# Optimization experiments

Measured on AMD Instinct MI355X. Metric: run time of the kernel, lower is better.

Reference implementation:

```python
import jax, jax.numpy as jnp
import numpy as np
from jax import lax

B, C, H, W = 8, 128, 64, 64
L = H * W  # 4096, multiple of 64 so BiMamba2's pad-to-chunk is a no-op
DM, DI, DS, DC, NH, HD = 32, 64, 64, 4, 1, 64  # d_model, d_inner, d_state, d_conv, nheads, headdim


def setup_inputs() -> dict:
    key = jax.random.key(0)
    ks = jax.random.split(key, 12)
    def r(i, shape, s):
        return jax.random.normal(ks[i], shape, jnp.float32) * s
    return {
        "x": jax.random.normal(ks[0], (B, C, H, W), jnp.float32),
        "lin1_w": r(1, (C, C), 0.05), "lin1_b": jnp.zeros((C,), jnp.float32),
        "dw_w": r(2, (C, 1, 3, 3), 0.1), "dw_b": jnp.zeros((C,), jnp.float32),
        "fc_in_w": r(3, (C, DM), 0.05),
        "mam_in_w": r(4, (2, DM, 2 * DI + 2 * DS + NH), 0.05),
        "mam_conv_w": r(5, (2, DI + 2 * DS, DC), 0.1),
        "mam_conv_b": jnp.zeros((2, DI + 2 * DS), jnp.float32),
        "mam_dt_bias": r(6, (2, NH), 0.1),
        "mam_A_log": jnp.zeros((2, NH), jnp.float32),
        "mam_D": jnp.ones((2, NH), jnp.float32),
        "mam_norm_w": jnp.ones((2, DI), jnp.float32),
        "mam_out_w": r(7, (2, DI, DM), 0.05),
        "fc_out_w": r(8, (DM, C), 0.05),
        "bn_g": jnp.ones((C,), jnp.float32), "bn_b": jnp.zeros((C,), jnp.float32),
        "conv4_w": r(9, (C, C), 0.05), "conv4_b": jnp.zeros((C,), jnp.float32),
    }


def _causal_dwconv1d(x, w, b):
    # x: (B, L, Ch); w: (Ch, DC) depthwise causal kernel (torch Conv1d groups=Ch, pad=DC-1, trimmed)
    xc = jnp.transpose(x, (0, 2, 1))
    xc = jnp.pad(xc, ((0, 0), (0, 0), (DC - 1, 0)))
    o = lax.conv_general_dilated(xc, w[:, None, :], (1,), "VALID",
                                 feature_group_count=w.shape[0],
                                 dimension_numbers=("NCH", "OIH", "NCH"))
    return jnp.transpose(o + b[None, :, None], (0, 2, 1))


def _mamba2(u, W_in, conv_w, conv_b, dt_bias, A_log, D, norm_w, W_out):
    # u: (B, L, DM). Minimal Mamba2 block: in_proj -> causal dwconv/silu -> selective scan -> gated RMSNorm -> out_proj
    b, l, _ = u.shape
    zxbcdt = u @ W_in                         # (b, l, 2*DI + 2*DS + NH)
    z = zxbcdt[..., :DI]
    xBC = zxbcdt[..., DI:DI + DI + 2 * DS]
    dt = zxbcdt[..., -NH:]
    xBC = jax.nn.silu(_causal_dwconv1d(xBC, conv_w, conv_b))
    xs = xBC[..., :DI]
    Bm = xBC[..., DI:DI + DS]                 # (b, l, DS)
    Cm = xBC[..., DI + DS:]                   # (b, l, DS)
    dt = jax.nn.softplus(dt + dt_bias)        # (b, l, NH)
    dA = jnp.exp(dt * (-jnp.exp(A_log)))      # (b, l, NH)
    xh = xs.reshape(b, l, NH, HD)
    dtx = dt[..., None] * xh                  # (b, l, NH, HD)

    def step(h, inp):
        dA_t, dtx_t, B_t, C_t = inp
        h = dA_t[:, :, None, None] * h + dtx_t[..., None] * B_t[:, None, None, :]
        y = jnp.einsum("bhpn,bn->bhp", h, C_t)
        return h, y

    h0 = jnp.zeros((b, NH, HD, DS), u.dtype)
    _, ys = lax.scan(step, h0, (jnp.moveaxis(dA, 1, 0), jnp.moveaxis(dtx, 1, 0),
                                jnp.moveaxis(Bm, 1, 0), jnp.moveaxis(Cm, 1, 0)))
    y = jnp.moveaxis(ys, 0, 1) + D[None, None, :, None] * xh   # (b, l, NH, HD)
    y = y.reshape(b, l, DI)
    y = y * jax.nn.silu(z)                    # gated RMSNorm
    y = y * lax.rsqrt(jnp.mean(y * y, -1, keepdims=True) + 1e-5) * norm_w
    return y @ W_out                          # (b, l, DM)


def _forward(x, lin1_w, lin1_b, dw_w, dw_b, fc_in_w, mam_in_w, mam_conv_w, mam_conv_b,
             mam_dt_bias, mam_A_log, mam_D, mam_norm_w, mam_out_w, fc_out_w,
             bn_g, bn_b, conv4_w, conv4_b):
    b, c, h, w = x.shape
    o = jnp.einsum("bihw,io->bohw", x, lin1_w) + lin1_b[None, :, None, None]
    o = lax.conv_general_dilated(o, dw_w, (1, 1), "SAME", feature_group_count=c,
                                 dimension_numbers=("NCHW", "OIHW", "NCHW")) + dw_b[None, :, None, None]
    o = jax.nn.silu(o)
    # BiMamba2_2D: flatten HxW -> sequence, fc_in, forward + reversed Mamba2, fc_out
    s = jnp.einsum("bcl,cd->bld", o.reshape(b, c, h * w), fc_in_w)
    y1 = _mamba2(s, mam_in_w[0], mam_conv_w[0], mam_conv_b[0], mam_dt_bias[0],
                 mam_A_log[0], mam_D[0], mam_norm_w[0], mam_out_w[0])
    y2 = jnp.flip(_mamba2(jnp.flip(s, 1), mam_in_w[1], mam_conv_w[1], mam_conv_b[1],
                          mam_dt_bias[1], mam_A_log[1], mam_D[1], mam_norm_w[1], mam_out_w[1]), 1)
    o = jnp.transpose((y1 + y2) @ fc_out_w, (0, 2, 1)).reshape(b, c, h, w)
    # BatchNorm2d (training-mode batch statistics)
    mu = jnp.mean(o, (0, 2, 3), keepdims=True)
    var = jnp.mean((o - mu) ** 2, (0, 2, 3), keepdims=True)
    o = (o - mu) * lax.rsqrt(var + 1e-5) * bn_g[None, :, None, None] + bn_b[None, :, None, None]
    g = jax.nn.sigmoid(jnp.einsum("bihw,io->bohw", o, conv4_w) + conv4_b[None, :, None, None])
    return g * x + x


def reference(x, lin1_w, lin1_b, dw_w, dw_b, fc_in_w, mam_in_w, mam_conv_w, mam_conv_b,
              mam_dt_bias, mam_A_log, mam_D, mam_norm_w, mam_out_w, fc_out_w,
              bn_g, bn_b, conv4_w, conv4_b):
    return _forward(x, lin1_w, lin1_b, dw_w, dw_b, fc_in_w, mam_in_w, mam_conv_w, mam_conv_b,
                    mam_dt_bias, mam_A_log, mam_D, mam_norm_w, mam_out_w, fc_out_w,
                    bn_g, bn_b, conv4_w, conv4_b)
```

## Files before the change

kernel.cpp:

```cpp
#include <hip/hip_runtime.h>
#include <math.h>

constexpr int Bn = 8, Cn = 128, Ln = 4096;

constexpr size_t OFF_O1   = 0;
constexpr size_t OFF_O2   = 4194304;
constexpr size_t OFF_S    = 8388608;
constexpr size_t OFF_Z    = 9437184;
constexpr size_t OFF_WT   = 11534336;
constexpr size_t OFF_XBCA = 13631488;
constexpr size_t OFF_DTS  = 26214400;
constexpr size_t OFF_CUM  = 26279936;
constexpr size_t OFF_T    = 26345472;
constexpr size_t OFF_SPREV= 30539776;
constexpr size_t OFF_S2A  = 34734080;
constexpr size_t OFF_S2B  = 35782656;
constexpr size_t OFF_BN   = 36831232;
constexpr size_t OFF_O3   = 0;

constexpr long XSTRIDE_H = 6291456;
constexpr long TSTRIDE = 2097152;

typedef __attribute__((ext_vector_type(8))) short short8;
typedef __attribute__((ext_vector_type(4))) float f32x4;
typedef __attribute__((ext_vector_type(4))) unsigned short us4;

__device__ __forceinline__ float siluf(float v) { return v / (1.0f + expf(-v)); }

__device__ __forceinline__ unsigned short tobf(float f) {
  unsigned int u = __float_as_uint(f);
  u += 0x7FFFu + ((u >> 16) & 1u);
  return (unsigned short)(u >> 16);
}

__device__ __forceinline__ float frombf(unsigned short u) {
  return __uint_as_float(((unsigned int)u) << 16);
}

__device__ __forceinline__ short8 ldfrag(const unsigned short* p) {
  union { unsigned int u[4]; short8 s; } cv;
  cv.u[0] = *(const unsigned int*)(p);
  cv.u[1] = *(const unsigned int*)(p + 2);
  cv.u[2] = *(const unsigned int*)(p + 4);
  cv.u[3] = *(const unsigned int*)(p + 6);
  return cv.s;
}

__global__ void k_prepW(const float* __restrict__ Win, unsigned short* __restrict__ WT) {
  int dir = blockIdx.x, tid = threadIdx.x;
  for (int idx = tid; idx < 272 * 32; idx += 256) {
    int n = idx >> 5, kk = idx & 31;
    float v = (n < 257) ? Win[dir * 32 * 257 + kk * 257 + n] : 0.f;
    WT[dir * 8704 + idx] = tobf(v);
  }
}

__global__ __launch_bounds__(256) void k_lin1(const float* __restrict__ x,
                                              const float* __restrict__ w,
                                              const float* __restrict__ bias,
                                              float* __restrict__ o1) {
  __shared__ unsigned short wT[64][140];
  __shared__ unsigned short xT[64][140];
  int b = blockIdx.y, l0 = blockIdx.x * 64, cb = blockIdx.z * 64;
  int tid = threadIdx.x, lane = tid & 63, mt = tid >> 6;
  int q = lane >> 4, i = lane & 15;
  int c4 = (tid & 15) * 4, k0 = tid >> 4;
#pragma unroll
  for (int s = 0; s < 8; ++s) {
    int k = k0 + s * 16;
    float4 wv = *(const float4*)&w[k * 128 + cb + c4];
    wT[c4 + 0][k] = tobf(wv.x); wT[c4 + 1][k] = tobf(wv.y);
    wT[c4 + 2][k] = tobf(wv.z); wT[c4 + 3][k] = tobf(wv.w);
    float4 xv = *(const float4*)&x[((long)b * 128 + k) * 4096 + l0 + c4];
    xT[c4 + 0][k] = tobf(xv.x); xT[c4 + 1][k] = tobf(xv.y);
    xT[c4 + 2][k] = tobf(xv.z); xT[c4 + 3][k] = tobf(xv.w);
  }
  __syncthreads();
  short8 af[4];
#pragma unroll
  for (int kk = 0; kk < 4; ++kk)
    af[kk] = ldfrag(&wT[mt * 16 + i][q * 8 + 32 * kk]);
  float bv[4];
#pragma unroll
  for (int r2 = 0; r2 < 4; ++r2) bv[r2] = bias[cb + 16 * mt + q * 4 + r2];
#pragma unroll
  for (int nt = 0; nt < 4; ++nt) {
    f32x4 d = {0.f, 0.f, 0.f, 0.f};
#pragma unroll
    for (int kk = 0; kk < 4; ++kk) {
      short8 bfr = ldfrag(&xT[nt * 16 + i][q * 8 + 32 * kk]);
      d = __builtin_amdgcn_mfma_f32_16x16x32_bf16(af[kk], bfr, d, 0, 0, 0);
    }
#pragma unroll
    for (int r2 = 0; r2 < 4; ++r2) {
      int c = 16 * mt + q * 4 + r2;
      o1[((long)b * 128 + cb + c) * 4096 + l0 + nt * 16 + i] = d[r2] + bv[r2];
    }
  }
}

__global__ void k_dw(const float* __restrict__ o1, const float* __restrict__ wgt,
                     const float* __restrict__ bias, float* __restrict__ o2) {
  __shared__ float p[4096];
  int bc = blockIdx.x, c = bc & 127, tid = threadIdx.x;
  const float* src = o1 + (long)bc * 4096;
#pragma unroll
  for (int s4 = 0; s4 < 4; ++s4) {
    int off = s4 * 1024 + tid * 4;
    *(float4*)&p[off] = *(const float4*)&src[off];
  }
  float wr[9];
#pragma unroll
  for (int j = 0; j < 9; ++j) wr[j] = wgt[c * 9 + j];
  float bv = bias[c];
  __syncthreads();
  int wg = tid & 15, hs = tid >> 4;
  int w0 = wg * 4, h0 = hs * 4;
  float in[6][6];
#pragma unroll
  for (int ri = 0; ri < 6; ++ri) {
    int h = h0 - 1 + ri;
    if (h < 0 || h > 63) {
#pragma unroll
      for (int ci = 0; ci < 6; ++ci) in[ri][ci] = 0.f;
    } else {
      float4 cc = *(float4*)&p[h * 64 + w0];
      in[ri][1] = cc.x; in[ri][2] = cc.y; in[ri][3] = cc.z; in[ri][4] = cc.w;
      in[ri][0] = (w0 > 0) ? p[h * 64 + w0 - 1] : 0.f;
      in[ri][5] = (w0 < 60) ? p[h * 64 + w0 + 4] : 0.f;
    }
  }
#pragma unroll
  for (int r = 0; r < 4; ++r) {
    float oc[4];
#pragma unroll
    for (int q = 0; q < 4; ++q) {
      float acc = bv;
#pragma unroll
      for (int dh = 0; dh < 3; ++dh)
#pragma unroll
        for (int dq = 0; dq < 3; ++dq)
          acc += in[r + dh][q + dq] * wr[dh * 3 + dq];
      oc[q] = siluf(acc);
    }
    *(float4*)&o2[(long)bc * 4096 + (h0 + r) * 64 + w0] =
        make_float4(oc[0], oc[1], oc[2], oc[3]);
  }
}

__global__ void k_fcin(const float* __restrict__ o2, const float* __restrict__ w,
                       unsigned short* __restrict__ sb) {
  __shared__ float xt[128][64];
  __shared__ float wt[128][32];
  int b = blockIdx.y, l0 = blockIdx.x * 64;
  int tid = threadIdx.x;
  int f4 = (tid & 15) * 4, r0 = tid >> 4;
#pragma unroll
  for (int st = 0; st < 8; ++st) {
    int r = r0 + st * 16;
    *(float4*)&xt[r][f4] = *(const float4*)&o2[((long)b * 128 + r) * 4096 + l0 + f4];
  }
  int f4w = (tid & 7) * 4, rw = tid >> 3;
#pragma unroll
  for (int st = 0; st < 4; ++st) {
    int r = rw + st * 32;
    *(float4*)&wt[r][f4w] = *(const float4*)&w[r * 32 + f4w];
  }
  __syncthreads();
  int tx = tid & 15, ty = tid >> 4;
  int c0 = tx * 4, d0 = ty * 2;
  float acc[2][4] = {};
  for (int k = 0; k < 128; ++k) {
    float4 xv = *(float4*)&xt[k][c0];
    float2 wv = *(float2*)&wt[k][d0];
    float xa[4] = {xv.x, xv.y, xv.z, xv.w};
#pragma unroll
    for (int q = 0; q < 4; ++q) {
      acc[0][q] += wv.x * xa[q];
      acc[1][q] += wv.y * xa[q];
    }
  }
#pragma unroll
  for (int q = 0; q < 4; ++q) {
    long ob = ((long)b * 4096 + l0 + c0 + q) * 32 + d0;
    unsigned int pk = (unsigned int)tobf(acc[0][q]) |
                      ((unsigned int)tobf(acc[1][q]) << 16);
    *(unsigned int*)&sb[ob] = pk;
  }
}

__global__ __launch_bounds__(256) void k_inprojconv(
    const unsigned short* __restrict__ sb, const unsigned short* __restrict__ WT,
    const float* __restrict__ conv_w, const float* __restrict__ conv_b,
    const float* __restrict__ dt_bias, const float* __restrict__ A_log,
    unsigned short* __restrict__ zT, unsigned short* __restrict__ xbca,
    float* __restrict__ dts, float* __restrict__ cum) {
  __shared__ unsigned short xbcT[192][82];
  __shared__ float dtL[64];
  int dir = blockIdx.z, b = blockIdx.y, l0 = blockIdx.x * 64;
  int tid = threadIdx.x, lane = tid & 63, mt = tid >> 6;
  int q = lane >> 4, i = lane & 15;
  long rowbase = (long)b * 4096 + l0;
  const unsigned short* W = WT + (long)dir * 8704;
  const short8 zfrag = {0, 0, 0, 0, 0, 0, 0, 0};

  if (mt == 0) {
    short8 afr[4];
#pragma unroll
    for (int rt = 0; rt < 4; ++rt) {
      int l = l0 + 16 * rt + i;
      int lsrc = dir ? (4095 - l) : l;
      afr[rt] = *(const short8*)&sb[((long)b * 4096 + lsrc) * 32 + q * 8];
    }
#pragma unroll
    for (int ct = 0; ct < 4; ++ct) {
      int n = 16 * ct + i;
      short8 bfr = *(const short8*)&W[n * 32 + q * 8];
      unsigned short* zrow = zT + (((long)dir * 64 + n) * 8 + b) * 4096 + l0 + q * 4;
#pragma unroll
      for (int rt = 0; rt < 4; ++rt) {
        f32x4 d = {0.f, 0.f, 0.f, 0.f};
        d = __builtin_amdgcn_mfma_f32_16x16x32_bf16(afr[rt], bfr, d, 0, 0, 0);
        us4 pk;
        pk[0] = tobf(d[0]); pk[1] = tobf(d[1]);
        pk[2] = tobf(d[2]); pk[3] = tobf(d[3]);
        *(us4*)&zrow[16 * rt] = pk;
      }
    }
    {
      short8 bfr = *(const short8*)&W[(256 + i) * 32 + q * 8];
#pragma unroll
      for (int rt = 0; rt < 4; ++rt) {
        f32x4 d = {0.f, 0.f, 0.f, 0.f};
        d = __builtin_amdgcn_mfma_f32_16x16x32_bf16(afr[rt], bfr, d, 0, 0, 0);
        if (i == 0) {
#pragma unroll
          for (int r2 = 0; r2 < 4; ++r2) dtL[16 * rt + q * 4 + r2] = d[r2];
        }
      }
    }
  } else {
    short8 afr[5];
#pragma unroll
    for (int rt = 0; rt < 5; ++rt) {
      int l = l0 - 3 + 16 * rt + i;
      if (l >= 0 && l < 4096) {
        int lsrc = dir ? (4095 - l) : l;
        afr[rt] = *(const short8*)&sb[((long)b * 4096 + lsrc) * 32 + q * 8];
      } else {
        afr[rt] = zfrag;
      }
    }
#pragma unroll
    for (int cti = 0; cti < 4; ++cti) {
      int n = 16 * (mt * 4 + cti) + i;
      short8 bfr = *(const short8*)&W[n * 32 + q * 8];
      int cc = n - 64;
#pragma unroll
      for (int rt = 0; rt < 5; ++rt) {
        f32x4 d = {0.f, 0.f, 0.f, 0.f};
        d = __builtin_amdgcn_mfma_f32_16x16x32_bf16(afr[rt], bfr, d, 0, 0, 0);
        int rr0 = 16 * rt + q * 4;
        unsigned int p0 = (unsigned int)tobf(d[0]) | ((unsigned int)tobf(d[1]) << 16);
        unsigned int p1 = (unsigned int)tobf(d[2]) | ((unsigned int)tobf(d[3]) << 16);
        *(unsigned int*)&xbcT[cc][rr0] = p0;
        *(unsigned int*)&xbcT[cc][rr0 + 2] = p1;
      }
    }
  }
  __syncthreads();

  if (tid < 192) {
    int c = tid;
    float cw0 = conv_w[dir * 768 + c * 4 + 0];
    float cw1 = conv_w[dir * 768 + c * 4 + 1];
    float cw2 = conv_w[dir * 768 + c * 4 + 2];
    float cw3 = conv_w[dir * 768 + c * 4 + 3];
    float cb2 = conv_b[dir * 192 + c];
    unsigned short* xp = xbca + (long)dir * XSTRIDE_H;
    float win0 = 0.f, win1 = 0.f, win2 = 0.f, win3 = 0.f;
    for (int rp = 0; rp < 34; ++rp) {
      unsigned int pk = *(const unsigned int*)&xbcT[c][rp * 2];
      float a0 = frombf((unsigned short)(pk & 0xFFFFu));
      float a1 = frombf((unsigned short)(pk >> 16));
      int rr = rp * 2;
      win0 = win1; win1 = win2; win2 = win3; win3 = a0;
      if (rr >= 3 && rr <= 66) {
        float acc = cb2 + win0 * cw0 + win1 * cw1 + win2 * cw2 + win3 * cw3;
        xp[(rowbase + rr - 3) * 192 + c] = tobf(siluf(acc));
      }
      win0 = win1; win1 = win2; win2 = win3; win3 = a1;
      if (rr + 1 >= 3 && rr + 1 <= 66) {
        float acc = cb2 + win0 * cw0 + win1 * cw1 + win2 * cw2 + win3 * cw3;
        xp[(rowbase + rr - 2) * 192 + c] = tobf(siluf(acc));
      }
    }
  } else {
    int ln = tid - 192;
    float v = dtL[ln] + dt_bias[dir];
    float sp = (v > 20.f) ? v : log1pf(expf(v));
    dts[dir * 32768 + rowbase + ln] = sp;
    float cd = -expf(A_log[dir]) * sp;
#pragma unroll
    for (int off = 1; off < 64; off <<= 1) {
      float u = __shfl_up(cd, off);
      if (ln >= off) cd += u;
    }
    cum[dir * 32768 + rowbase + ln] = cd;
  }
}

__global__ void k_chunkT(const unsigned short* __restrict__ xbca,
                         const float* __restrict__ dts,
                         const float* __restrict__ cum, float* __restrict__ T) {
  __shared__ float Xs[64][68], Bs[64][68];
  int dir = blockIdx.y;
  int bk = blockIdx.x, b = bk >> 6, k = bk & 63;
  int tid = threadIdx.x;
  const unsigned short* xp = xbca + (long)dir * XSTRIDE_H;
  const float* dtp = dts + dir * 32768;
  const float* cp = cum + dir * 32768;
  long base = (long)b * 4096 + (long)k * 64;
  float clend = cp[base + 63];
  {
    int c4 = (tid & 15) * 4, r0 = tid >> 4;
#pragma unroll
    for (int s = 0; s < 4; ++s) {
      int r = r0 + s * 16;
      float f = expf(clend - cp[base + r]) * dtp[base + r];
      const unsigned short* rowp = &xp[(base + r) * 192];
      us4 xv = *(const us4*)&rowp[c4];
      us4 bv = *(const us4*)&rowp[64 + c4];
#pragma unroll
      for (int j = 0; j < 4; ++j) {
        Xs[r][c4 + j] = frombf(xv[j]) * f;
        Bs[r][c4 + j] = frombf(bv[j]);
      }
    }
  }
  __syncthreads();
  int tx = tid & 15, ty = tid >> 4;
  int p0 = ty * 4, n0 = tx * 4;
  float acc[4][4] = {};
  for (int s = 0; s < 64; ++s) {
    float4 xv = *(float4*)&Xs[s][p0];
    float4 bv = *(float4*)&Bs[s][n0];
    float xa[4] = {xv.x, xv.y, xv.z, xv.w};
    float ba[4] = {bv.x, bv.y, bv.z, bv.w};
#pragma unroll
    for (int a = 0; a < 4; ++a)
#pragma unroll
      for (int q = 0; q < 4; ++q) acc[a][q] += xa[a] * ba[q];
  }
#pragma unroll
  for (int a = 0; a < 4; ++a)
    *(float4*)&T[(long)dir * TSTRIDE + (long)bk * 4096 + (p0 + a) * 64 + n0] =
        make_float4(acc[a][0], acc[a][1], acc[a][2], acc[a][3]);
}

__global__ void k_scan(const float* __restrict__ T, const float* __restrict__ cum,
                       float* __restrict__ Sprev) {
  __shared__ float E[64];
  int blk = blockIdx.x;
  int dirb = blk >> 4;
  int dir = dirb >> 3, b = dirb & 7;
  int pn = (blk & 15) * 256 + threadIdx.x;
  const float* cp = cum + dir * 32768 + b * 4096;
  if (threadIdx.x < 64) E[threadIdx.x] = expf(cp[threadIdx.x * 64 + 63]);
  __syncthreads();
  const float* Tp = T + (long)dir * TSTRIDE + (long)b * 262144 + pn;
  float* Sp = Sprev + (long)dir * TSTRIDE + (long)b * 262144 + pn;
  float sacc = 0.f;
  float tb[16];
#pragma unroll
  for (int j = 0; j < 16; ++j) tb[j] = Tp[(long)j * 4096];
  for (int kc = 0; kc < 4; ++kc) {
    float tn[16];
    if (kc < 3) {
#pragma unroll
      for (int j = 0; j < 16; ++j) tn[j] = Tp[(long)(kc * 16 + 16 + j) * 4096];
    }
#pragma unroll
    for (int j = 0; j < 16; ++j) {
      int k = kc * 16 + j;
      Sp[(long)k * 4096] = sacc;
      sacc = fmaf(E[k], sacc, tb[j]);
    }
    if (kc < 3) {
#pragma unroll
      for (int j = 0; j < 16; ++j) tb[j] = tn[j];
    }
  }
}

__global__ __launch_bounds__(256) void k_chunkYout(
    const unsigned short* __restrict__ xbca, const float* __restrict__ dts,
    const float* __restrict__ cum, const float* __restrict__ Sprev,
    const float* __restrict__ Dp, const unsigned short* __restrict__ zT,
    const float* __restrict__ normw, const float* __restrict__ Wout,
    float* __restrict__ s2a, float* __restrict__ s2b) {
  __shared__ unsigned short Cb[64][72];
  __shared__ unsigned short Bop[64][68];
  __shared__ unsigned short Gb[64][72];
  __shared__ unsigned short WnT[32][66];
  __shared__ float cumS[64];
  int dir = blockIdx.y;
  int bk = blockIdx.x, b = bk >> 6, k = bk & 63;
  int tid = threadIdx.x, lane = tid & 63, mt = tid >> 6;
  int q = lane >> 4, i = lane & 15;
  const unsigned short* xp = xbca + (long)dir * XSTRIDE_H;
  const float* dtp = dts + dir * 32768;
  const float* cp = cum + dir * 32768;
  const float* Sp = Sprev + (long)dir * TSTRIDE;
  long base = (long)b * 4096 + (long)k * 64;

  {
    int c4 = (tid & 15) * 4, r0 = tid >> 4;
#pragma unroll
    for (int s = 0; s < 4; ++s) {
      int r = r0 + s * 16;
      float dtv = dtp[base + r];
      const unsigned short* rowp = &xp[(base + r) * 192 + 64];
      us4 bv = *(const us4*)&rowp[c4];
      us4 cv = *(const us4*)&rowp[64 + c4];
      us4 bo;
#pragma unroll
      for (int j = 0; j < 4; ++j) bo[j] = tobf(frombf(bv[j]) * dtv);
      *(us4*)&Bop[r][c4] = bo;
      *(us4*)&Cb[r][c4] = cv;
    }
  }
  for (int idx = tid; idx < 2048; idx += 256) {
    int p = idx >> 5, d = idx & 31;
    WnT[d][p] = tobf(normw[dir * 64 + p] * Wout[(long)dir * 2048 + p * 32 + d]);
  }
  if (tid < 64) cumS[tid] = cp[base + tid];
  __syncthreads();

  short8 a0 = *(const short8*)&Cb[mt * 16 + i][q * 8];
  short8 a1 = *(const short8*)&Cb[mt * 16 + i][q * 8 + 32];

#pragma unroll
  for (int lt = 0; lt < 4; ++lt) {
    short8 b0 = ldfrag(&Bop[lt * 16 + i][q * 8]);
    short8 b1 = ldfrag(&Bop[lt * 16 + i][q * 8 + 32]);
    f32x4 d = {0.f, 0.f, 0.f, 0.f};
    d = __builtin_amdgcn_mfma_f32_16x16x32_bf16(a0, b0, d, 0, 0, 0);
    d = __builtin_amdgcn_mfma_f32_16x16x32_bf16(a1, b1, d, 0, 0, 0);
#pragma unroll
    for (int r2 = 0; r2 < 4; ++r2) {
      int t = mt * 16 + q * 4 + r2;
      int l = lt * 16 + i;
      float g = (l <= t) ? d[r2] * expf(cumS[t] - cumS[l]) : 0.f;
      Gb[t][l] = tobf(g);
    }
  }
  __syncthreads();

  {
    int c4 = (tid & 15) * 4, r0 = tid >> 4;
#pragma unroll
    for (int s = 0; s < 4; ++s) {
      int r = r0 + s * 16;
      float4 sv = *(const float4*)&Sp[(long)bk * 4096 + r * 64 + c4];
      us4 bo;
      bo[0] = tobf(sv.x); bo[1] = tobf(sv.y);
      bo[2] = tobf(sv.z); bo[3] = tobf(sv.w);
      *(us4*)&Bop[r][c4] = bo;
    }
  }
  __syncthreads();

  f32x4 dint[4];
#pragma unroll
  for (int lt = 0; lt < 4; ++lt) {
    short8 b0 = ldfrag(&Bop[lt * 16 + i][q * 8]);
    short8 b1 = ldfrag(&Bop[lt * 16 + i][q * 8 + 32]);
    f32x4 d = {0.f, 0.f, 0.f, 0.f};
    d = __builtin_amdgcn_mfma_f32_16x16x32_bf16(a0, b0, d, 0, 0, 0);
    d = __builtin_amdgcn_mfma_f32_16x16x32_bf16(a1, b1, d, 0, 0, 0);
    dint[lt] = d;
  }
  __syncthreads();

#pragma unroll
  for (int j = 0; j < 8; ++j) {
    int s = mt * 16 + 2 * j;
    unsigned int pk = (unsigned int)xp[(base + s) * 192 + lane] |
                      ((unsigned int)xp[(base + s + 1) * 192 + lane] << 16);
    *(unsigned int*)&Bop[lane][s] = pk;
  }
  __syncthreads();

  short8 g0 = *(const short8*)&Gb[mt * 16 + i][q * 8];
  short8 g1 = *(const short8*)&Gb[mt * 16 + i][q * 8 + 32];
  float Dv = Dp[dir];
  float et4[4];
#pragma unroll
  for (int r2 = 0; r2 < 4; ++r2) et4[r2] = expf(cumS[mt * 16 + q * 4 + r2]);
  float yv[4][4];
  float rowss[4] = {0.f, 0.f, 0.f, 0.f};
#pragma unroll
  for (int lt = 0; lt < 4; ++lt) {
    short8 b0 = ldfrag(&Bop[lt * 16 + i][q * 8]);
    short8 b1 = ldfrag(&Bop[lt * 16 + i][q * 8 + 32]);
    f32x4 d = {0.f, 0.f, 0.f, 0.f};
    d = __builtin_amdgcn_mfma_f32_16x16x32_bf16(g0, b0, d, 0, 0, 0);
    d = __builtin_amdgcn_mfma_f32_16x16x32_bf16(g1, b1, d, 0, 0, 0);
    us4 zq = *(const us4*)&zT[(((long)dir * 64 + lt * 16 + i) * 8 + b) * 4096 +
                              (long)k * 64 + mt * 16 + q * 4];
    unsigned int xpk0 = *(const unsigned int*)&Bop[lt * 16 + i][mt * 16 + q * 4];
    unsigned int xpk1 = *(const unsigned int*)&Bop[lt * 16 + i][mt * 16 + q * 4 + 2];
    float xvr[4];
    xvr[0] = frombf((unsigned short)(xpk0 & 0xFFFFu));
    xvr[1] = frombf((unsigned short)(xpk0 >> 16));
    xvr[2] = frombf((unsigned short)(xpk1 & 0xFFFFu));
    xvr[3] = frombf((unsigned short)(xpk1 >> 16));
#pragma unroll
    for (int r2 = 0; r2 < 4; ++r2) {
      float y = d[r2] + et4[r2] * dint[lt][r2] + Dv * xvr[r2];
      float zv = frombf(zq[r2]);
      float v = y * siluf(zv);
      yv[lt][r2] = v;
      rowss[r2] += v * v;
    }
  }
#pragma unroll
  for (int m = 1; m < 16; m <<= 1) {
#pragma unroll
    for (int r2 = 0; r2 < 4; ++r2) rowss[r2] += __shfl_xor(rowss[r2], m);
  }
  float rscv[4];
#pragma unroll
  for (int r2 = 0; r2 < 4; ++r2)
    rscv[r2] = rsqrtf(rowss[r2] * (1.0f / 64.0f) + 1e-5f);
#pragma unroll
  for (int lt = 0; lt < 4; ++lt)
#pragma unroll
    for (int r2 = 0; r2 < 4; ++r2) {
      int t = mt * 16 + q * 4 + r2;
      int p = lt * 16 + i;
      Gb[t][p] = tobf(yv[lt][r2] * rscv[r2]);
    }
  __syncthreads();

  short8 y0 = *(const short8*)&Gb[mt * 16 + i][q * 8];
  short8 y1 = *(const short8*)&Gb[mt * 16 + i][q * 8 + 32];
  float* s2x = dir ? s2b : s2a;
#pragma unroll
  for (int dt = 0; dt < 2; ++dt) {
    short8 b0 = ldfrag(&WnT[dt * 16 + i][q * 8]);
    short8 b1 = ldfrag(&WnT[dt * 16 + i][q * 8 + 32]);
    f32x4 d = {0.f, 0.f, 0.f, 0.f};
    d = __builtin_amdgcn_mfma_f32_16x16x32_bf16(y0, b0, d, 0, 0, 0);
    d = __builtin_amdgcn_mfma_f32_16x16x32_bf16(y1, b1, d, 0, 0, 0);
#pragma unroll
    for (int r2 = 0; r2 < 4; ++r2) {
      int tl = mt * 16 + q * 4 + r2;
      int l = k * 64 + tl;
      int lout = dir ? (4095 - l) : l;
      int dd = dt * 16 + i;
      s2x[((long)b * 4096 + lout) * 32 + dd] = d[r2];
    }
  }
}

__global__ void k_fcout(const float* __restrict__ s2a, const float* __restrict__ s2b,
                        const float* __restrict__ w, float* __restrict__ o3) {
  __shared__ float st[32][68];
  __shared__ float wt[32][64];
  int b = blockIdx.y, l0 = blockIdx.x * 64, cb = blockIdx.z * 64;
  int tid = threadIdx.x;
  {
    int d = tid & 31, l = tid >> 5;
    for (int si = 0; si < 8; ++si) {
      int ll = l + si * 8;
      long o = ((long)b * 4096 + l0 + ll) * 32 + d;
      st[d][ll] = s2a[o] + s2b[o];
    }
    int f4 = (tid & 15) * 4, r = tid >> 4;
    for (int si = 0; si < 2; ++si) {
      int rr = r + si * 16;
      *(float4*)&wt[rr][f4] = *(const float4*)&w[rr * 128 + cb + f4];
    }
  }
  __syncthreads();
  int tx = tid & 15, ty = tid >> 4;
  int c0 = tx * 4, t0 = ty * 4;
  float acc[4][4] = {};
  for (int k = 0; k < 32; ++k) {
    float4 xv = *(float4*)&st[k][c0];
    float4 wv = *(float4*)&wt[k][t0];
    float xa[4] = {xv.x, xv.y, xv.z, xv.w};
    float wa[4] = {wv.x, wv.y, wv.z, wv.w};
#pragma unroll
    for (int a = 0; a < 4; ++a)
#pragma unroll
      for (int q = 0; q < 4; ++q) acc[a][q] += wa[a] * xa[q];
  }
#pragma unroll
  for (int a = 0; a < 4; ++a)
    *(float4*)&o3[((long)b * 128 + cb + t0 + a) * 4096 + l0 + c0] =
        make_float4(acc[a][0], acc[a][1], acc[a][2], acc[a][3]);
}

__global__ void k_bnstat(const float* __restrict__ o3, float* __restrict__ stats) {
  int bc = blockIdx.x;
  int tid = threadIdx.x;
  const float* p = o3 + (long)bc * 4096;
  float s = 0.f, q = 0.f;
  for (int i = tid * 4; i < 4096; i += 1024) {
    float4 v = *(const float4*)&p[i];
    s += v.x + v.y + v.z + v.w;
    q += v.x * v.x + v.y * v.y + v.z * v.z + v.w * v.w;
  }
  __shared__ float rs[4], rq[4];
  for (int off = 32; off; off >>= 1) { s += __shfl_down(s, off); q += __shfl_down(q, off); }
  if ((tid & 63) == 0) { rs[tid >> 6] = s; rq[tid >> 6] = q; }
  __syncthreads();
  if (tid == 0) {
    float a = rs[0] + rs[1] + rs[2] + rs[3];
    float b2 = rq[0] + rq[1] + rq[2] + rq[3];
    int c = bc & 127;
    atomicAdd(&stats[c], a);
    atomicAdd(&stats[128 + c], b2);
  }
}

__global__ __launch_bounds__(256) void k_final(const float* __restrict__ o3,
                                               const float* __restrict__ stats,
                                               const float* __restrict__ bng,
                                               const float* __restrict__ bnb,
                                               const float* __restrict__ w,
                                               const float* __restrict__ bias,
                                               const float* __restrict__ x,
                                               float* __restrict__ out) {
  __shared__ unsigned short wT[64][140];
  __shared__ unsigned short aT[64][140];
  __shared__ float sc[128], sh[128];
  int b = blockIdx.y, l0 = blockIdx.x * 64, cb = blockIdx.z * 64;
  int tid = threadIdx.x, lane = tid & 63, mt = tid >> 6;
  int q = lane >> 4, i = lane & 15;
  if (tid < 128) {
    float mu = stats[tid] * (1.0f / 32768.0f);
    float var = stats[128 + tid] * (1.0f / 32768.0f) - mu * mu;
    float r = rsqrtf(var + 1e-5f);
    sc[tid] = r * bng[tid];
    sh[tid] = bnb[tid] - mu * r * bng[tid];
  }
  __syncthreads();
  int c4 = (tid & 15) * 4, k0 = tid >> 4;
#pragma unroll
  for (int s = 0; s < 8; ++s) {
    int k = k0 + s * 16;
    float4 wv = *(const float4*)&w[k * 128 + cb + c4];
    wT[c4 + 0][k] = tobf(wv.x); wT[c4 + 1][k] = tobf(wv.y);
    wT[c4 + 2][k] = tobf(wv.z); wT[c4 + 3][k] = tobf(wv.w);
    float4 av = *(const float4*)&o3[((long)b * 128 + k) * 4096 + l0 + c4];
    float scr = sc[k], shr = sh[k];
    aT[c4 + 0][k] = tobf(fmaf(av.x, scr, shr));
    aT[c4 + 1][k] = tobf(fmaf(av.y, scr, shr));
    aT[c4 + 2][k] = tobf(fmaf(av.z, scr, shr));
    aT[c4 + 3][k] = tobf(fmaf(av.w, scr, shr));
  }
  __syncthreads();
  short8 af[4];
#pragma unroll
  for (int kk = 0; kk < 4; ++kk)
    af[kk] = ldfrag(&wT[mt * 16 + i][q * 8 + 32 * kk]);
  float bv[4];
#pragma unroll
  for (int r2 = 0; r2 < 4; ++r2) bv[r2] = bias[cb + 16 * mt + q * 4 + r2];
#pragma unroll
  for (int nt = 0; nt < 4; ++nt) {
    f32x4 d = {0.f, 0.f, 0.f, 0.f};
#pragma unroll
    for (int kk = 0; kk < 4; ++kk) {
      short8 bfr = ldfrag(&aT[nt * 16 + i][q * 8 + 32 * kk]);
      d = __builtin_amdgcn_mfma_f32_16x16x32_bf16(af[kk], bfr, d, 0, 0, 0);
    }
#pragma unroll
    for (int r2 = 0; r2 < 4; ++r2) {
      int c = 16 * mt + q * 4 + r2;
      long xi = ((long)b * 128 + cb + c) * 4096 + l0 + nt * 16 + i;
      float g = 1.0f / (1.0f + expf(-(d[r2] + bv[r2])));
      out[xi] = x[xi] * (1.0f + g);
    }
  }
}

extern "C" void kernel_launch(void* const* d_in, const int* in_sizes, int n_in,
                              void* d_out, int out_size, void* d_ws, size_t ws_size,
                              hipStream_t stream) {
  const float* x          = (const float*)d_in[0];
  const float* lin1_w     = (const float*)d_in[1];
  const float* lin1_b     = (const float*)d_in[2];
  const float* dw_w       = (const float*)d_in[3];
  const float* dw_b       = (const float*)d_in[4];
  const float* fc_in_w    = (const float*)d_in[5];
  const float* mam_in_w   = (const float*)d_in[6];
  const float* mam_conv_w = (const float*)d_in[7];
  const float* mam_conv_b = (const float*)d_in[8];
  const float* mam_dt_bias= (const float*)d_in[9];
  const float* mam_A_log  = (const float*)d_in[10];
  const float* mam_D      = (const float*)d_in[11];
  const float* mam_norm_w = (const float*)d_in[12];
  const float* mam_out_w  = (const float*)d_in[13];
  const float* fc_out_w   = (const float*)d_in[14];
  const float* bn_g       = (const float*)d_in[15];
  const float* bn_b       = (const float*)d_in[16];
  const float* conv4_w    = (const float*)d_in[17];
  const float* conv4_b    = (const float*)d_in[18];
  float* out = (float*)d_out;
  float* ws  = (float*)d_ws;

  float* o1   = ws + OFF_O1;
  float* o2   = ws + OFF_O2;
  unsigned short* sbuf = (unsigned short*)(ws + OFF_S);
  unsigned short* zTb  = (unsigned short*)(ws + OFF_Z);
  unsigned short* WTb  = (unsigned short*)(ws + OFF_WT);
  unsigned short* xbca = (unsigned short*)(ws + OFF_XBCA);
  float* dts  = ws + OFF_DTS;
  float* cum  = ws + OFF_CUM;
  float* Tbuf = ws + OFF_T;
  float* Sprev= ws + OFF_SPREV;
  float* s2a  = ws + OFF_S2A;
  float* s2b  = ws + OFF_S2B;
  float* bnst = ws + OFF_BN;
  float* o3   = ws + OFF_O3;

  hipMemsetAsync(bnst, 0, 256 * sizeof(float), stream);

  k_prepW<<<2, 256, 0, stream>>>(mam_in_w, WTb);
  k_lin1<<<dim3(64, 8, 2), 256, 0, stream>>>(x, lin1_w, lin1_b, o1);
  k_dw<<<1024, 256, 0, stream>>>(o1, dw_w, dw_b, o2);
  k_fcin<<<dim3(64, 8), 256, 0, stream>>>(o2, fc_in_w, sbuf);
  k_inprojconv<<<dim3(64, 8, 2), 256, 0, stream>>>(sbuf, WTb, mam_conv_w, mam_conv_b,
                                                   mam_dt_bias, mam_A_log,
                                                   zTb, xbca, dts, cum);
  k_chunkT<<<dim3(512, 2), 256, 0, stream>>>(xbca, dts, cum, Tbuf);
  k_scan<<<256, 256, 0, stream>>>(Tbuf, cum, Sprev);
  k_chunkYout<<<dim3(512, 2), 256, 0, stream>>>(xbca, dts, cum, Sprev, mam_D, zTb,
                                                mam_norm_w, mam_out_w, s2a, s2b);
  k_fcout<<<dim3(64, 8, 2), 256, 0, stream>>>(s2a, s2b, fc_out_w, o3);
  k_bnstat<<<1024, 256, 0, stream>>>(o3, bnst);
  k_final<<<dim3(64, 8, 2), 256, 0, stream>>>(o3, bnst, bn_g, bn_b, conv4_w, conv4_b, x, out);
}
```

Baseline: 223.7 us.

## Fuse chunk-state GEMM into inproj, fold BN stats into fcout, bf16 Sprev

```diff
diff --git a/kernel.cpp b/kernel.cpp
--- a/kernel.cpp
+++ b/kernel.cpp
@@ -46,15 +46,6 @@
   return cv.s;
 }
 
-__global__ void k_prepW(const float* __restrict__ Win, unsigned short* __restrict__ WT) {
-  int dir = blockIdx.x, tid = threadIdx.x;
-  for (int idx = tid; idx < 272 * 32; idx += 256) {
-    int n = idx >> 5, kk = idx & 31;
-    float v = (n < 257) ? Win[dir * 32 * 257 + kk * 257 + n] : 0.f;
-    WT[dir * 8704 + idx] = tobf(v);
-  }
-}
-
 __global__ __launch_bounds__(256) void k_lin1(const float* __restrict__ x,
                                               const float* __restrict__ w,
                                               const float* __restrict__ bias,
@@ -149,7 +140,8 @@
 }
 
 __global__ void k_fcin(const float* __restrict__ o2, const float* __restrict__ w,
-                       unsigned short* __restrict__ sb) {
+                       unsigned short* __restrict__ sb,
+                       const float* __restrict__ Win, unsigned short* __restrict__ WT) {
   __shared__ float xt[128][64];
   __shared__ float wt[128][32];
   int b = blockIdx.y, l0 = blockIdx.x * 64;
@@ -187,6 +179,14 @@
                       ((unsigned int)tobf(acc[1][q]) << 16);
     *(unsigned int*)&sb[ob] = pk;
   }
+  if (blockIdx.y == 0 && blockIdx.x < 2) {
+    int dir = blockIdx.x;
+    for (int idx = tid; idx < 272 * 32; idx += 256) {
+      int n = idx >> 5, kk = idx & 31;
+      float v = (n < 257) ? Win[dir * 32 * 257 + kk * 257 + n] : 0.f;
+      WT[dir * 8704 + idx] = tobf(v);
+    }
+  }
 }
 
 __global__ __launch_bounds__(256) void k_inprojconv(
@@ -194,9 +194,11 @@
     const float* __restrict__ conv_w, const float* __restrict__ conv_b,
     const float* __restrict__ dt_bias, const float* __restrict__ A_log,
     unsigned short* __restrict__ zT, unsigned short* __restrict__ xbca,
-    float* __restrict__ dts, float* __restrict__ cum) {
+    float* __restrict__ dts, float* __restrict__ cum, float* __restrict__ Tg) {
   __shared__ unsigned short xbcT[192][82];
+  __shared__ float fXf[64][68];
   __shared__ float dtL[64];
+  __shared__ float dtsS[64], cumSS[64], fL[64];
   int dir = blockIdx.z, b = blockIdx.y, l0 = blockIdx.x * 64;
   int tid = threadIdx.x, lane = tid & 63, mt = tid >> 6;
   int q = lane >> 4, i = lane & 15;
@@ -287,12 +289,20 @@
       win0 = win1; win1 = win2; win2 = win3; win3 = a0;
       if (rr >= 3 && rr <= 66) {
         float acc = cb2 + win0 * cw0 + win1 * cw1 + win2 * cw2 + win3 * cw3;
-        xp[(rowbase + rr - 3) * 192 + c] = tobf(siluf(acc));
+        float sv = siluf(acc);
+        int t = rr - 3;
+        xp[(rowbase + t) * 192 + c] = tobf(sv);
+        if (c < 64) fXf[c][t] = sv;
+        else if (c < 128) xbcT[c][t] = tobf(sv);
       }
       win0 = win1; win1 = win2; win2 = win3; win3 = a1;
       if (rr + 1 >= 3 && rr + 1 <= 66) {
         float acc = cb2 + win0 * cw0 + win1 * cw1 + win2 * cw2 + win3 * cw3;
-        xp[(rowbase + rr - 2) * 192 + c] = tobf(siluf(acc));
+        float sv = siluf(acc);
+        int t = rr - 2;
+        xp[(rowbase + t) * 192 + c] = tobf(sv);
+        if (c < 64) fXf[c][t] = sv;
+        else if (c < 128) xbcT[c][t] = tobf(sv);
       }
     }
   } else {
@@ -300,6 +310,7 @@
     float v = dtL[ln] + dt_bias[dir];
     float sp = (v > 20.f) ? v : log1pf(expf(v));
     dts[dir * 32768 + rowbase + ln] = sp;
+    dtsS[ln] = sp;
     float cd = -expf(A_log[dir]) * sp;
 #pragma unroll
     for (int off = 1; off < 64; off <<= 1) {
@@ -307,84 +318,74 @@
       if (ln >= off) cd += u;
     }
     cum[dir * 32768 + rowbase + ln] = cd;
-  }
-}
-
-__global__ void k_chunkT(const unsigned short* __restrict__ xbca,
-                         const float* __restrict__ dts,
-                         const float* __restrict__ cum, float* __restrict__ T) {
-  __shared__ float Xs[64][68], Bs[64][68];
-  int dir = blockIdx.y;
-  int bk = blockIdx.x, b = bk >> 6, k = bk & 63;
-  int tid = threadIdx.x;
-  const unsigned short* xp = xbca + (long)dir * XSTRIDE_H;
-  const float* dtp = dts + dir * 32768;
-  const float* cp = cum + dir * 32768;
-  long base = (long)b * 4096 + (long)k * 64;
-  float clend = cp[base + 63];
+    cumSS[ln] = cd;
+  }
+  __syncthreads();
+
+  if (tid < 64) fL[tid] = expf(cumSS[63] - cumSS[tid]) * dtsS[tid];
+  __syncthreads();
+
   {
-    int c4 = (tid & 15) * 4, r0 = tid >> 4;
-#pragma unroll
-    for (int s = 0; s < 4; ++s) {
-      int r = r0 + s * 16;
-      float f = expf(clend - cp[base + r]) * dtp[base + r];
-      const unsigned short* rowp = &xp[(base + r) * 192];
-      us4 xv = *(const us4*)&rowp[c4];
-      us4 bv = *(const us4*)&rowp[64 + c4];
-#pragma unroll
-      for (int j = 0; j < 4; ++j) {
-        Xs[r][c4 + j] = frombf(xv[j]) * f;
-        Bs[r][c4 + j] = frombf(bv[j]);
-      }
-    }
-  }
-  __syncthreads();
-  int tx = tid & 15, ty = tid >> 4;
-  int p0 = ty * 4, n0 = tx * 4;
-  float acc[4][4] = {};
-  for (int s = 0; s < 64; ++s) {
-    float4 xv = *(float4*)&Xs[s][p0];
-    float4 bv = *(float4*)&Bs[s][n0];
-    float xa[4] = {xv.x, xv.y, xv.z, xv.w};
-    float ba[4] = {bv.x, bv.y, bv.z, bv.w};
-#pragma unroll
-    for (int a = 0; a < 4; ++a)
-#pragma unroll
-      for (int q = 0; q < 4; ++q) acc[a][q] += xa[a] * ba[q];
-  }
-#pragma unroll
-  for (int a = 0; a < 4; ++a)
-    *(float4*)&T[(long)dir * TSTRIDE + (long)bk * 4096 + (p0 + a) * 64 + n0] =
-        make_float4(acc[a][0], acc[a][1], acc[a][2], acc[a][3]);
+    int c = tid & 63, tb2 = (tid >> 6) * 16;
+#pragma unroll
+    for (int j = 0; j < 8; ++j) {
+      int t = tb2 + 2 * j;
+      float2 v = *(const float2*)&fXf[c][t];
+      unsigned int pk = (unsigned int)tobf(v.x * fL[t]) |
+                        ((unsigned int)tobf(v.y * fL[t + 1]) << 16);
+      *(unsigned int*)&xbcT[c][t] = pk;
+    }
+  }
+  __syncthreads();
+
+  {
+    short8 a0 = ldfrag(&xbcT[mt * 16 + i][q * 8]);
+    short8 a1 = ldfrag(&xbcT[mt * 16 + i][q * 8 + 32]);
+    float* Tp = Tg + (long)dir * TSTRIDE + ((long)(b * 64 + blockIdx.x)) * 4096;
+#pragma unroll
+    for (int nt = 0; nt < 4; ++nt) {
+      short8 b0 = ldfrag(&xbcT[64 + nt * 16 + i][q * 8]);
+      short8 b1 = ldfrag(&xbcT[64 + nt * 16 + i][q * 8 + 32]);
+      f32x4 d = {0.f, 0.f, 0.f, 0.f};
+      d = __builtin_amdgcn_mfma_f32_16x16x32_bf16(a0, b0, d, 0, 0, 0);
+      d = __builtin_amdgcn_mfma_f32_16x16x32_bf16(a1, b1, d, 0, 0, 0);
+#pragma unroll
+      for (int r2 = 0; r2 < 4; ++r2)
+        Tp[(mt * 16 + q * 4 + r2) * 64 + nt * 16 + i] = d[r2];
+    }
+  }
 }
 
 __global__ void k_scan(const float* __restrict__ T, const float* __restrict__ cum,
-                       float* __restrict__ Sprev) {
+                       unsigned short* __restrict__ Sprev) {
   __shared__ float E[64];
   int blk = blockIdx.x;
-  int dirb = blk >> 4;
+  int dirb = blk >> 3;
   int dir = dirb >> 3, b = dirb & 7;
-  int pn = (blk & 15) * 256 + threadIdx.x;
+  int pn = (blk & 7) * 512 + threadIdx.x * 2;
   const float* cp = cum + dir * 32768 + b * 4096;
   if (threadIdx.x < 64) E[threadIdx.x] = expf(cp[threadIdx.x * 64 + 63]);
   __syncthreads();
   const float* Tp = T + (long)dir * TSTRIDE + (long)b * 262144 + pn;
-  float* Sp = Sprev + (long)dir * TSTRIDE + (long)b * 262144 + pn;
-  float sacc = 0.f;
-  float tb[16];
-#pragma unroll
-  for (int j = 0; j < 16; ++j) tb[j] = Tp[(long)j * 4096];
+  unsigned short* Sp = Sprev + (long)dir * TSTRIDE + (long)b * 262144 + pn;
+  float s0 = 0.f, s1 = 0.f;
+  float2 tb[16];
+#pragma unroll
+  for (int j = 0; j < 16; ++j) tb[j] = *(const float2*)&Tp[(long)j * 4096];
   for (int kc = 0; kc < 4; ++kc) {
-    float tn[16];
+    float2 tn[16];
     if (kc < 3) {
 #pragma unroll
-      for (int j = 0; j < 16; ++j) tn[j] = Tp[(long)(kc * 16 + 16 + j) * 4096];
+      for (int j = 0; j < 16; ++j)
+        tn[j] = *(const float2*)&Tp[(long)(kc * 16 + 16 + j) * 4096];
     }
 #pragma unroll
     for (int j = 0; j < 16; ++j) {
       int k = kc * 16 + j;
-      Sp[(long)k * 4096] = sacc;
-      sacc = fmaf(E[k], sacc, tb[j]);
+      unsigned int pk = (unsigned int)tobf(s0) | ((unsigned int)tobf(s1) << 16);
+      *(unsigned int*)&Sp[(long)k * 4096] = pk;
+      s0 = fmaf(E[k], s0, tb[j].x);
+      s1 = fmaf(E[k], s1, tb[j].y);
     }
     if (kc < 3) {
 #pragma unroll
@@ -395,7 +396,7 @@
 
 __global__ __launch_bounds__(256) void k_chunkYout(
     const unsigned short* __restrict__ xbca, const float* __restrict__ dts,
-    const float* __restrict__ cum, const float* __restrict__ Sprev,
+    const float* __restrict__ cum, const unsigned short* __restrict__ Sprev,
     const float* __restrict__ Dp, const unsigned short* __restrict__ zT,
     const float* __restrict__ normw, const float* __restrict__ Wout,
     float* __restrict__ s2a, float* __restrict__ s2b) {
@@ -411,7 +412,7 @@
   const unsigned short* xp = xbca + (long)dir * XSTRIDE_H;
   const float* dtp = dts + dir * 32768;
   const float* cp = cum + dir * 32768;
-  const float* Sp = Sprev + (long)dir * TSTRIDE;
+  const unsigned short* Sp = Sprev + (long)dir * TSTRIDE;
   long base = (long)b * 4096 + (long)k * 64;
 
   {
@@ -462,11 +463,8 @@
 #pragma unroll
     for (int s = 0; s < 4; ++s) {
       int r = r0 + s * 16;
-      float4 sv = *(const float4*)&Sp[(long)bk * 4096 + r * 64 + c4];
-      us4 bo;
-      bo[0] = tobf(sv.x); bo[1] = tobf(sv.y);
-      bo[2] = tobf(sv.z); bo[3] = tobf(sv.w);
-      *(us4*)&Bop[r][c4] = bo;
+      us4 sv = *(const us4*)&Sp[(long)bk * 4096 + r * 64 + c4];
+      *(us4*)&Bop[r][c4] = sv;
     }
   }
   __syncthreads();
@@ -566,7 +564,8 @@
 }
 
 __global__ void k_fcout(const float* __restrict__ s2a, const float* __restrict__ s2b,
-                        const float* __restrict__ w, float* __restrict__ o3) {
+                        const float* __restrict__ w, float* __restrict__ o3,
+                        float* __restrict__ stats) {
   __shared__ float st[32][68];
   __shared__ float wt[32][64];
   int b = blockIdx.y, l0 = blockIdx.x * 64, cb = blockIdx.z * 64;
@@ -602,28 +601,28 @@
   for (int a = 0; a < 4; ++a)
     *(float4*)&o3[((long)b * 128 + cb + t0 + a) * 4096 + l0 + c0] =
         make_float4(acc[a][0], acc[a][1], acc[a][2], acc[a][3]);
-}
-
-__global__ void k_bnstat(const float* __restrict__ o3, float* __restrict__ stats) {
-  int bc = blockIdx.x;
-  int tid = threadIdx.x;
-  const float* p = o3 + (long)bc * 4096;
-  float s = 0.f, q = 0.f;
-  for (int i = tid * 4; i < 4096; i += 1024) {
-    float4 v = *(const float4*)&p[i];
-    s += v.x + v.y + v.z + v.w;
-    q += v.x * v.x + v.y * v.y + v.z * v.z + v.w * v.w;
-  }
-  __shared__ float rs[4], rq[4];
-  for (int off = 32; off; off >>= 1) { s += __shfl_down(s, off); q += __shfl_down(q, off); }
-  if ((tid & 63) == 0) { rs[tid >> 6] = s; rq[tid >> 6] = q; }
-  __syncthreads();
-  if (tid == 0) {
-    float a = rs[0] + rs[1] + rs[2] + rs[3];
-    float b2 = rq[0] + rq[1] + rq[2] + rq[3];
-    int c = bc & 127;
-    atomicAdd(&stats[c], a);
-    atomicAdd(&stats[128 + c], b2);
+  float ssum[4], sqq[4];
+#pragma unroll
+  for (int a = 0; a < 4; ++a) {
+    ssum[a] = acc[a][0] + acc[a][1] + acc[a][2] + acc[a][3];
+    sqq[a] = acc[a][0] * acc[a][0] + acc[a][1] * acc[a][1] +
+             acc[a][2] * acc[a][2] + acc[a][3] * acc[a][3];
+  }
+#pragma unroll
+  for (int m = 1; m < 16; m <<= 1) {
+#pragma unroll
+    for (int a = 0; a < 4; ++a) {
+      ssum[a] += __shfl_xor(ssum[a], m);
+      sqq[a] += __shfl_xor(sqq[a], m);
+    }
+  }
+  if (tx == 0) {
+#pragma unroll
+    for (int a = 0; a < 4; ++a) {
+      int ch = cb + t0 + a;
+      atomicAdd(&stats[ch], ssum[a]);
+      atomicAdd(&stats[128 + ch], sqq[a]);
+    }
   }
 }
 
@@ -723,7 +722,7 @@
   float* dts  = ws + OFF_DTS;
   float* cum  = ws + OFF_CUM;
   float* Tbuf = ws + OFF_T;
-  float* Sprev= ws + OFF_SPREV;
+  unsigned short* Sprev = (unsigned short*)(ws + OFF_SPREV);
   float* s2a  = ws + OFF_S2A;
   float* s2b  = ws + OFF_S2B;
   float* bnst = ws + OFF_BN;
@@ -731,18 +730,15 @@
 
   hipMemsetAsync(bnst, 0, 256 * sizeof(float), stream);
 
-  k_prepW<<<2, 256, 0, stream>>>(mam_in_w, WTb);
   k_lin1<<<dim3(64, 8, 2), 256, 0, stream>>>(x, lin1_w, lin1_b, o1);
   k_dw<<<1024, 256, 0, stream>>>(o1, dw_w, dw_b, o2);
-  k_fcin<<<dim3(64, 8), 256, 0, stream>>>(o2, fc_in_w, sbuf);
+  k_fcin<<<dim3(64, 8), 256, 0, stream>>>(o2, fc_in_w, sbuf, mam_in_w, WTb);
   k_inprojconv<<<dim3(64, 8, 2), 256, 0, stream>>>(sbuf, WTb, mam_conv_w, mam_conv_b,
                                                    mam_dt_bias, mam_A_log,
-                                                   zTb, xbca, dts, cum);
-  k_chunkT<<<dim3(512, 2), 256, 0, stream>>>(xbca, dts, cum, Tbuf);
-  k_scan<<<256, 256, 0, stream>>>(Tbuf, cum, Sprev);
+                                                   zTb, xbca, dts, cum, Tbuf);
+  k_scan<<<128, 256, 0, stream>>>(Tbuf, cum, Sprev);
   k_chunkYout<<<dim3(512, 2), 256, 0, stream>>>(xbca, dts, cum, Sprev, mam_D, zTb,
                                                 mam_norm_w, mam_out_w, s2a, s2b);
-  k_fcout<<<dim3(64, 8, 2), 256, 0, stream>>>(s2a, s2b, fc_out_w, o3);
-  k_bnstat<<<1024, 256, 0, stream>>>(o3, bnst);
+  k_fcout<<<dim3(64, 8, 2), 256, 0, stream>>>(s2a, s2b, fc_out_w, o3, bnst);
   k_final<<<dim3(64, 8, 2), 256, 0, stream>>>(o3, bnst, bn_g, bn_b, conv4_w, conv4_b, x, out);
 }
```

New measurement: 271.6 us. +21.4%, slower.
